# Optimization experiments

Measured on AMD Instinct MI355X. Metric: run time of the kernel, lower is better.

## Reference

```python
import jax, jax.numpy as jnp
import numpy as np

B, NN, D, H, L, E, NC = 512, 64, 128, 4, 2, 262144, 8
N = B * NN
HD = D // H


def _mlp(x, W1, b1, W2, b2):
    return jax.nn.relu(x @ W1 + b1) @ W2 + b2


def setup_inputs() -> dict:
    key = jax.random.key(0)
    ks = iter(jax.random.split(key, 64))
    w = lambda shape, s=0.02: jax.random.normal(next(ks), shape, dtype=jnp.float32) * s
    inp = {
        'node_features': jax.random.randint(next(ks), (N,), 0, NC, dtype=jnp.int32),
        'edge_index': jax.random.randint(next(ks), (2, E), 0, N, dtype=jnp.int32),
        'ptr': jnp.arange(B + 1, dtype=jnp.int32) * NN,
        'node_emb_table': w((NC, D), 1.0),
        'edge_emb': jnp.clip(jax.random.normal(next(ks), (1, D), dtype=jnp.float32), -2.0, 2.0),
        'eW1': w((L, 3 * D, D)), 'eb1': jnp.zeros((L, D)), 'eW2': w((L, D, D)), 'eb2': jnp.zeros((L, D)),
        'nW1': w((L, 3 * D, D)), 'nb1': jnp.zeros((L, D)), 'nW2': w((L, D, D)), 'nb2': jnp.zeros((L, D)),
        'gW1': w((L, 3 * D, D)), 'gb1': jnp.zeros((L, D)), 'gW2': w((L, D, D)), 'gb2': jnp.zeros((L, D)),
        'projW': w((D, 3 * D)), 'projb': jnp.zeros((3 * D,)),
        'Wq': w((D, D)), 'Wk': w((D, D)), 'Wv': w((D, D)),
        'bq': jnp.zeros((D,)), 'bk': jnp.zeros((D,)), 'bv': jnp.zeros((D,)),
        'outW': w((D, D)), 'outb': jnp.zeros((D,)),
        'sW1': w((D, D)), 'sb1': jnp.zeros((D,)), 'sW2': w((D, D)), 'sb2': jnp.zeros((D,)),
        'rW1': w((D, D)), 'rb1': jnp.zeros((D,)), 'rW2': w((D, D)), 'rb2': jnp.zeros((D,)),
        'stW1': w((D, D)), 'stb1': jnp.zeros((D,)), 'stW2': w((D, 1)), 'stb2': jnp.zeros((1,)),
        'temperature': jnp.float32(1.0),
    }
    return inp


def reference(node_features, edge_index, ptr, node_emb_table, edge_emb,
              eW1, eb1, eW2, eb2, nW1, nb1, nW2, nb2, gW1, gb1, gW2, gb2,
              projW, projb, Wq, Wk, Wv, bq, bk, bv, outW, outb,
              sW1, sb1, sW2, sb2, rW1, rb1, rW2, rb2,
              stW1, stb1, stW2, stb2, temperature):
    n_graphs = ptr.shape[0] - 1                       # static
    batch_idx = jnp.repeat(jnp.arange(n_graphs), NN)  # uniform graphs of NN nodes
    node_embs = node_emb_table[node_features]         # [N, D]
    edge_embs = jnp.broadcast_to(edge_emb, (edge_index.shape[1], D))  # [E, D]
    g = jnp.zeros((n_graphs, D), node_embs.dtype)
    src, dst = edge_index[0], edge_index[1]
    for l in range(L):
        ein = jnp.concatenate([node_embs[src], node_embs[dst], edge_embs], -1)  # [E, 3D]
        edge_embs = edge_embs + _mlp(ein, eW1[l], eb1[l], eW2[l], eb2[l])
        node_aggr = jax.ops.segment_sum(edge_embs, dst, num_segments=N)         # [N, D]
        nin = jnp.concatenate([node_embs, node_aggr, g[batch_idx]], -1)
        node_embs = node_embs + _mlp(nin, nW1[l], nb1[l], nW2[l], nb2[l])
        eg = jax.ops.segment_sum(node_aggr, batch_idx, num_segments=n_graphs)
        ng = jax.ops.segment_sum(node_embs, batch_idx, num_segments=n_graphs)
        g = g + _mlp(jnp.concatenate([ng, eg, g], -1), gW1[l], gb1[l], gW2[l], gb2[l])
    # projection + self-attention over the NN nodes of each graph
    x = node_embs.reshape(n_graphs, NN, D) @ projW + projb   # [B, NN, 3D]
    q, k, v = jnp.split(x, 3, axis=-1)
    qh = (q @ Wq + bq).reshape(n_graphs, NN, H, HD)
    kh = (k @ Wk + bk).reshape(n_graphs, NN, H, HD)
    vh = (v @ Wv + bv).reshape(n_graphs, NN, H, HD)
    scores = jnp.einsum('bqhd,bkhd->bhqk', qh, kh) / jnp.sqrt(jnp.float32(HD))
    attn = jax.nn.softmax(scores, axis=-1)
    ctx = jnp.einsum('bhqk,bkhd->bqhd', attn, vh).reshape(n_graphs, NN, D)
    a = ctx @ outW + outb
    senders = _mlp(a, sW1, sb1, sW2, sb2)
    receivers = _mlp(a, rW1, rb1, rW2, rb2)
    edge_actions = jnp.einsum('bqd,bkd->bqk', senders, receivers).reshape(n_graphs, NN * NN)
    edge_actions = edge_actions / jax.nn.softplus(temperature)
    stop = _mlp(g, stW1, stb1, stW2, stb2)[:, 0]
    at = jnp.full((n_graphs, 3), -jnp.inf, dtype=edge_actions.dtype)
    at = at.at[:, 1].set(jax.nn.log_sigmoid(-stop))   # ADD_EDGE
    at = at.at[:, 2].set(jax.nn.log_sigmoid(stop))    # EXIT
    return (at, edge_actions)
```

## Files before the change

### kernel.cpp

```cpp
#include <hip/hip_runtime.h>
#include <hip/hip_bf16.h>
#include <cstdint>
#include <cstddef>

#define D_   128
#define NN_  64
#define B_   512
#define N_   32768
#define E_   262144

typedef float4 f4;
typedef _Float16 h16;
typedef __attribute__((ext_vector_type(8))) _Float16 h16x8;
typedef __attribute__((ext_vector_type(4))) float f32x4;

__device__ __forceinline__ f4 ld4(const float* p) { return *(const f4*)p; }
__device__ __forceinline__ void st4(float* p, f4 v) { *(f4*)p = v; }

__device__ __forceinline__ int swz(int row, int slot) {
  return row * 128 + ((slot ^ (row & 7)) << 3);
}
__device__ __forceinline__ h16x8 pk8(f4 a, f4 b) {
  h16x8 v;
  v[0]=(h16)a.x; v[1]=(h16)a.y; v[2]=(h16)a.z; v[3]=(h16)a.w;
  v[4]=(h16)b.x; v[5]=(h16)b.y; v[6]=(h16)b.z; v[7]=(h16)b.w;
  return v;
}
#define MFMA16(a,b,c) __builtin_amdgcn_mfma_f32_16x16x32_f16((a),(b),(c),0,0,0)

__device__ __forceinline__ void stage_a32(const float* __restrict__ A, h16* A_s, int r0, int tid) {
  int r = tid >> 2, q = tid & 3;
  const float* Ar = A + (size_t)(r0 + r) * 128 + q * 32;
#pragma unroll
  for (int i = 0; i < 4; ++i)
    *(h16x8*)&A_s[swz(r, q * 4 + i)] = pk8(ld4(Ar + i * 8), ld4(Ar + i * 8 + 4));
}
__device__ __forceinline__ void stage_a16(const h16* __restrict__ A, h16* A_s, int r0, int tid) {
  int r = tid >> 2, q = tid & 3;
  const h16* Ar = A + (size_t)(r0 + r) * 128 + q * 32;
#pragma unroll
  for (int i = 0; i < 4; ++i)
    *(h16x8*)&A_s[swz(r, q * 4 + i)] = *(const h16x8*)(Ar + i * 8);
}
__device__ __forceinline__ void bfrag_g(const h16* __restrict__ Bt, int n0, int lq, int lr, h16x8 bf[2][4]) {
#pragma unroll
  for (int nf = 0; nf < 2; ++nf) {
    const h16* row = Bt + (size_t)(n0 + nf * 16 + lr) * 128 + lq * 8;
#pragma unroll
    for (int ks = 0; ks < 4; ++ks)
      bf[nf][ks] = *(const h16x8*)(row + ks * 32);
  }
}
__device__ __forceinline__ void mfma8(const h16* A_s, h16x8 bf[2][4], f32x4 acc[4][2], int lq, int lr) {
#pragma unroll
  for (int mf = 0; mf < 4; ++mf)
#pragma unroll
    for (int ks = 0; ks < 4; ++ks) {
      h16x8 af = *(h16x8*)&A_s[swz(mf * 16 + lr, ks * 4 + lq)];
      acc[mf][0] = MFMA16(af, bf[0][ks], acc[mf][0]);
      acc[mf][1] = MFMA16(af, bf[1][ks], acc[mf][1]);
    }
}
__device__ __forceinline__ void zacc(f32x4 acc[4][2]) {
#pragma unroll
  for (int mf = 0; mf < 4; ++mf) { acc[mf][0] = (f32x4)0.f; acc[mf][1] = (f32x4)0.f; }
}

__global__ __launch_bounds__(256)
void k_embed(const int* __restrict__ nf, const float* __restrict__ tab, float* __restrict__ out) {
  int idx = blockIdx.x * 256 + threadIdx.x;
  int row = idx >> 5, q = idx & 31;
  st4(out + (size_t)row * D_ + q * 4, ld4(tab + (size_t)nf[row] * D_ + q * 4));
}

__global__ __launch_bounds__(256)
void k_zero_cnt(int* __restrict__ cnt) { cnt[blockIdx.x * 256 + threadIdx.x] = 0; }

__global__ __launch_bounds__(256)
void k_hist(const int* __restrict__ dst, int* __restrict__ cnt) {
  atomicAdd(&cnt[dst[blockIdx.x * 256 + threadIdx.x]], 1);
}

__global__ __launch_bounds__(256)
void k_scan(const int* __restrict__ cnt, int* __restrict__ base, int* __restrict__ cursor) {
  __shared__ int sums[256];
  __shared__ int offs[256];
  const int t = threadIdx.x;
  const int start = t * 128;
  int s = 0;
  for (int i = 0; i < 128; ++i) s += cnt[start + i];
  sums[t] = s;
  __syncthreads();
  if (t == 0) { int acc = 0; for (int i = 0; i < 256; ++i) { offs[i] = acc; acc += sums[i]; } }
  __syncthreads();
  int off = offs[t];
  for (int i = 0; i < 128; ++i) { base[start + i] = off; cursor[start + i] = off; off += cnt[start + i]; }
  if (t == 255) base[N_] = off;
}

__global__ __launch_bounds__(256)
void k_scatter(const int* __restrict__ dst, int* __restrict__ cursor, int* __restrict__ eid) {
  int e = blockIdx.x * 256 + threadIdx.x;
  int p = atomicAdd(&cursor[dst[e]], 1);
  eid[p] = e;
}

__global__ __launch_bounds__(256)
void k_aggr(const h16* __restrict__ edgeb, const int* __restrict__ csrB,
            float* __restrict__ aggr) {
  const int node = blockIdx.x * 4 + (threadIdx.x >> 6);
  const int d2 = (threadIdx.x & 63) * 2;
  const int b0 = csrB[node], b1 = csrB[node + 1];
  float s0 = 0.f, s1 = 0.f;
  for (int i = b0; i < b1; ++i) {
    const h16* p = edgeb + (size_t)i * 128 + d2;
    s0 += (float)p[0]; s1 += (float)p[1];
  }
  aggr[(size_t)node * 128 + d2 + 0] = s0;
  aggr[(size_t)node * 128 + d2 + 1] = s1;
}

struct TP { const float* p[32]; };
__global__ __launch_bounds__(256)
void k_w2t(TP tp, h16* __restrict__ dst) {
  __shared__ h16 w_s[128][132];
  const float* S = tp.p[blockIdx.x];
  h16* Dd = dst + (size_t)blockIdx.x * 16384;
  const int t = threadIdx.x, r = t >> 1, hf = t & 1;
  for (int i = 0; i < 64; i += 4) {
    f4 x = ld4(S + r * 128 + hf * 64 + i);
    w_s[r][hf*64+i+0] = (h16)x.x; w_s[r][hf*64+i+1] = (h16)x.y;
    w_s[r][hf*64+i+2] = (h16)x.z; w_s[r][hf*64+i+3] = (h16)x.w;
  }
  __syncthreads();
  for (int i8 = 0; i8 < 64; i8 += 8) {
    h16x8 v;
#pragma unroll
    for (int j = 0; j < 8; ++j) v[j] = w_s[hf*64 + i8 + j][r];
    *(h16x8*)(Dd + (size_t)r * 128 + hf * 64 + i8) = v;
  }
}

__global__ __launch_bounds__(256, 2)
void k_weff(const float* __restrict__ projW, const h16* __restrict__ wt_qkv,
            h16* __restrict__ wout) {
  __shared__ h16 A_s[64 * 128];
  const int i = blockIdx.x >> 1, half = blockIdx.x & 1;
  const int r0 = half * 64;
  const int tid = threadIdx.x;
  const int lane = tid & 63, w = tid >> 6;
  const int n0 = w * 32, lq = lane >> 4, lr = lane & 15;
  stage_a16(wt_qkv + (size_t)i * 16384, A_s, r0, tid);
  __syncthreads();
  h16x8 bf[2][4];
#pragma unroll
  for (int nf = 0; nf < 2; ++nf) {
    const int r = n0 + nf * 16 + lr;
    const float* prow = projW + (size_t)r * 384 + i * 128 + lq * 8;
#pragma unroll
    for (int ks = 0; ks < 4; ++ks)
      bf[nf][ks] = pk8(ld4(prow + ks * 32), ld4(prow + ks * 32 + 4));
  }
  f32x4 acc[4][2];
  zacc(acc);
  mfma8(A_s, bf, acc, lq, lr);
  h16* Wo = wout + (size_t)i * 16384;
#pragma unroll
  for (int nf = 0; nf < 2; ++nf) {
    const int r = n0 + nf * 16 + lr;
#pragma unroll
    for (int mf = 0; mf < 4; ++mf)
#pragma unroll
      for (int reg = 0; reg < 4; ++reg)
        Wo[(size_t)(r0 + mf * 16 + lq * 4 + reg) * 128 + r] = (h16)acc[mf][nf][reg];
  }
}

__global__ __launch_bounds__(256, 2)
void k_gemm3o(const float* __restrict__ A,
              const h16* __restrict__ B1, const h16* __restrict__ B2,
              const h16* __restrict__ B3,
              const float* __restrict__ bias,
              h16* __restrict__ O1, h16* __restrict__ O2, h16* __restrict__ O3) {
  __shared__ h16 A_s[64 * 128];
  const int tid = threadIdx.x;
  const int r0 = blockIdx.x * 64;
  const int lane = tid & 63, w = tid >> 6;
  const int n0 = w * 32, lq = lane >> 4, lr = lane & 15;
  stage_a32(A, A_s, r0, tid);
  __syncthreads();
  const h16* Bs[3] = {B1, B2, B3};
  h16*       Os[3] = {O1, O2, O3};
#pragma unroll
  for (int o = 0; o < 3; ++o) {
    if (!Bs[o]) break;
    h16x8 bf[2][4];
    f32x4 acc[4][2];
    bfrag_g(Bs[o], n0, lq, lr, bf);
    zacc(acc);
    mfma8(A_s, bf, acc, lq, lr);
#pragma unroll
    for (int nf = 0; nf < 2; ++nf) {
      const int col = n0 + nf * 16 + lr;
      const float bv = bias ? bias[o * 128 + col] : 0.f;
#pragma unroll
      for (int mf = 0; mf < 4; ++mf)
#pragma unroll
        for (int reg = 0; reg < 4; ++reg)
          Os[o][(size_t)(r0 + mf * 16 + lq * 4 + reg) * 128 + col] = (h16)(acc[mf][nf][reg] + bv);
    }
  }
}

__global__ __launch_bounds__(256, 2)
void k_mlp2(const float* __restrict__ A1, const float* __restrict__ A2,
            const float* __restrict__ A3,
            const h16* __restrict__ B1a, const h16* __restrict__ B1b,
            const h16* __restrict__ B1c,
            const float* __restrict__ bias1,
            const h16* __restrict__ B2, const float* __restrict__ bias2,
            const float* __restrict__ addC,
            float* __restrict__ C) {
  __shared__ h16 A_s[64 * 128];
  const int tid = threadIdx.x;
  const int r0 = blockIdx.x * 64;
  const int lane = tid & 63, w = tid >> 6;
  const int n0 = w * 32, lq = lane >> 4, lr = lane & 15;
  h16x8 bf[2][4];
  f32x4 acc[4][2];
  zacc(acc);
  stage_a32(A1, A_s, r0, tid);
  __syncthreads();
  bfrag_g(B1a, n0, lq, lr, bf);
  mfma8(A_s, bf, acc, lq, lr);
  if (A2) {
    __syncthreads();
    stage_a32(A2, A_s, r0, tid);
    __syncthreads();
    bfrag_g(B1b, n0, lq, lr, bf);
    mfma8(A_s, bf, acc, lq, lr);
  }
  if (A3) {
    __syncthreads();
    stage_a32(A3, A_s, r0, tid);
    __syncthreads();
    bfrag_g(B1c, n0, lq, lr, bf);
    mfma8(A_s, bf, acc, lq, lr);
  }
  __syncthreads();
#pragma unroll
  for (int nf = 0; nf < 2; ++nf) {
    const int col = n0 + nf * 16 + lr;
    const float b1v = bias1 ? bias1[col] : 0.f;
#pragma unroll
    for (int mf = 0; mf < 4; ++mf)
#pragma unroll
      for (int reg = 0; reg < 4; ++reg) {
        const int row = mf * 16 + lq * 4 + reg;
        A_s[swz(row, col >> 3) + (col & 7)] = (h16)fmaxf(acc[mf][nf][reg] + b1v, 0.f);
      }
  }
  __syncthreads();
  bfrag_g(B2, n0, lq, lr, bf);
  zacc(acc);
  mfma8(A_s, bf, acc, lq, lr);
#pragma unroll
  for (int nf = 0; nf < 2; ++nf) {
    const int col = n0 + nf * 16 + lr;
    const float b2v = bias2 ? bias2[col] : 0.f;
#pragma unroll
    for (int mf = 0; mf < 4; ++mf)
#pragma unroll
      for (int reg = 0; reg < 4; ++reg) {
        const int row = r0 + mf * 16 + lq * 4 + reg;
        float x = acc[mf][nf][reg] + b2v;
        if (addC) x += addC[(size_t)row * 128 + col];
        C[(size_t)row * 128 + col] = x;
      }
  }
}

__global__ __launch_bounds__(256, 2)
void k_nodemlp(float* __restrict__ node, const float* __restrict__ aggr,
               const float* __restrict__ gbuf,
               const h16* __restrict__ B1a, const h16* __restrict__ B1b,
               const float* __restrict__ nW1c, const float* __restrict__ nb1,
               const h16* __restrict__ B2, const float* __restrict__ nb2,
               float* __restrict__ ngb, float* __restrict__ egb) {
  __shared__ h16 A_s[64 * 128];
  __shared__ float gt_s[2][128];
  __shared__ float eg_s[2][128];
  const int tid = threadIdx.x, g = blockIdx.x, r0 = g * 64;
  const int lane = tid & 63, w = tid >> 6;
  const int n0 = w * 32, lq = lane >> 4, lr = lane & 15;
  h16x8 bf[2][4];
  f32x4 acc[4][2];
  zacc(acc);
  stage_a32(node, A_s, r0, tid);
  __syncthreads();
  bfrag_g(B1a, n0, lq, lr, bf);
  mfma8(A_s, bf, acc, lq, lr);
  {
    const int col = tid & 127, half = tid >> 7;
    float s = 0.f;
    const float* gb = gbuf + (size_t)g * 128;
    for (int j = half * 64; j < half * 64 + 64; ++j)
      s += gb[j] * nW1c[(size_t)j * 128 + col];
    gt_s[half][col] = s;
  }
  __syncthreads();
  stage_a32(aggr, A_s, r0, tid);
  __syncthreads();
  bfrag_g(B1b, n0, lq, lr, bf);
  mfma8(A_s, bf, acc, lq, lr);
  {
    const int col = tid & 127, half = tid >> 7;
    float s = 0.f;
    for (int r = half * 32; r < half * 32 + 32; ++r)
      s += aggr[((size_t)r0 + r) * 128 + col];
    eg_s[half][col] = s;
  }
  __syncthreads();
#pragma unroll
  for (int nf = 0; nf < 2; ++nf) {
    const int col = n0 + nf * 16 + lr;
    const float gt = gt_s[0][col] + gt_s[1][col] + nb1[col];
#pragma unroll
    for (int mf = 0; mf < 4; ++mf)
#pragma unroll
      for (int reg = 0; reg < 4; ++reg) {
        const int row = mf * 16 + lq * 4 + reg;
        A_s[swz(row, col >> 3) + (col & 7)] = (h16)fmaxf(acc[mf][nf][reg] + gt, 0.f);
      }
  }
  if (tid < 128) egb[(size_t)g * 128 + tid] = eg_s[0][tid] + eg_s[1][tid];
  __syncthreads();
  bfrag_g(B2, n0, lq, lr, bf);
  zacc(acc);
  mfma8(A_s, bf, acc, lq, lr);
#pragma unroll
  for (int nf = 0; nf < 2; ++nf) {
    const int col = n0 + nf * 16 + lr;
    const float b2v = nb2[col];
    float cs = 0.f;
#pragma unroll
    for (int mf = 0; mf < 4; ++mf)
#pragma unroll
      for (int reg = 0; reg < 4; ++reg) {
        const int row = r0 + mf * 16 + lq * 4 + reg;
        float x = acc[mf][nf][reg] + b2v + node[(size_t)row * 128 + col];
        node[(size_t)row * 128 + col] = x;
        cs += x;
      }
    cs += __shfl_xor(cs, 16);
    cs += __shfl_xor(cs, 32);
    if (lq == 0) ngb[(size_t)g * 128 + col] = cs;
  }
}

__global__ __launch_bounds__(128)
void k_hc0(const float* __restrict__ ee, const float* __restrict__ W1c,
           const float* __restrict__ b1, float* __restrict__ hc0) {
  int j = threadIdx.x;
  float s = b1[j];
  for (int d = 0; d < 128; ++d) s += ee[d] * W1c[d * 128 + j];
  hc0[j] = s;
}

__global__ __launch_bounds__(256, 2)
void k_edge0(const int* __restrict__ src, const int* __restrict__ dst,
             const int* __restrict__ eid,
             const h16* __restrict__ hs, const h16* __restrict__ hd,
             const float* __restrict__ hc0, const h16* __restrict__ Wt2,
             const float* __restrict__ eb2, const float* __restrict__ ee,
             h16* __restrict__ edgeb) {
  __shared__ h16 H_s[64 * 128];
  __shared__ int ss[64], sd[64];
  const int tid = threadIdx.x;
  const int e0 = blockIdx.x * 64;
  const int lane = tid & 63, w = tid >> 6;
  const int n0 = w * 32, lq = lane >> 4, lr = lane & 15;
  if (tid < 64) { int e = eid[e0 + tid]; ss[tid] = src[e]; sd[tid] = dst[e]; }
  __syncthreads();
  {
    int e = tid >> 2, q = tid & 3;
    const h16* ps = hs + (size_t)ss[e] * 128 + q * 32;
    const h16* pd = hd + (size_t)sd[e] * 128 + q * 32;
#pragma unroll
    for (int i = 0; i < 4; ++i) {
      h16x8 a = *(const h16x8*)(ps + i * 8);
      h16x8 b = *(const h16x8*)(pd + i * 8);
      f4 c0 = ld4(hc0 + q * 32 + i * 8), c1 = ld4(hc0 + q * 32 + i * 8 + 4);
      h16x8 v;
      v[0]=(h16)fmaxf((float)a[0]+(float)b[0]+c0.x,0.f); v[1]=(h16)fmaxf((float)a[1]+(float)b[1]+c0.y,0.f);
      v[2]=(h16)fmaxf((float)a[2]+(float)b[2]+c0.z,0.f); v[3]=(h16)fmaxf((float)a[3]+(float)b[3]+c0.w,0.f);
      v[4]=(h16)fmaxf((float)a[4]+(float)b[4]+c1.x,0.f); v[5]=(h16)fmaxf((float)a[5]+(float)b[5]+c1.y,0.f);
      v[6]=(h16)fmaxf((float)a[6]+(float)b[6]+c1.z,0.f); v[7]=(h16)fmaxf((float)a[7]+(float)b[7]+c1.w,0.f);
      *(h16x8*)&H_s[swz(e, q * 4 + i)] = v;
    }
  }
  __syncthreads();
  h16x8 bf[2][4];
  f32x4 acc[4][2];
  bfrag_g(Wt2, n0, lq, lr, bf);
  zacc(acc);
  mfma8(H_s, bf, acc, lq, lr);
  __syncthreads();
#pragma unroll
  for (int nf = 0; nf < 2; ++nf) {
    const int col = n0 + nf * 16 + lr;
    const float base = eb2[col] + ee[col];
#pragma unroll
    for (int mf = 0; mf < 4; ++mf)
#pragma unroll
      for (int reg = 0; reg < 4; ++reg) {
        const int row = mf * 16 + lq * 4 + reg;
        H_s[swz(row, col >> 3) + (col & 7)] = (h16)(acc[mf][nf][reg] + base);
      }
  }
  __syncthreads();
  {
    int r = tid >> 2, q = tid & 3;
#pragma unroll
    for (int i = 0; i < 4; ++i) {
      int slot = q * 4 + i;
      h16x8 v = *(const h16x8*)&H_s[swz(r, slot)];
      *(h16x8*)(edgeb + (size_t)(e0 + r) * 128 + slot * 8) = v;
    }
  }
}

__global__ __launch_bounds__(256, 2)
void k_edge1(const int* __restrict__ src, const int* __restrict__ dst,
             const int* __restrict__ eid,
             h16* __restrict__ edgeb,
             const h16* __restrict__ hs, const h16* __restrict__ hd,
             const h16* __restrict__ Wt1c, const float* __restrict__ b1,
             const h16* __restrict__ Wt2, const float* __restrict__ b2) {
  __shared__ h16 T_s[64 * 128];
  __shared__ h16 HS_s[64 * 128];
  __shared__ int ss[64], sd[64];
  const int tid = threadIdx.x;
  const int e0 = blockIdx.x * 64;
  const int lane = tid & 63, w = tid >> 6;
  const int n0 = w * 32, lq = lane >> 4, lr = lane & 15;
  if (tid < 64) { int e = eid[e0 + tid]; ss[tid] = src[e]; sd[tid] = dst[e]; }
  {
    int r = tid >> 2, q = tid & 3;
    const h16* Er = edgeb + (size_t)(e0 + r) * 128 + q * 32;
#pragma unroll
    for (int i = 0; i < 4; ++i)
      *(h16x8*)&T_s[swz(r, q * 4 + i)] = *(const h16x8*)(Er + i * 8);
  }
  __syncthreads();
  {
    int e = tid >> 2, q = tid & 3;
    const h16* ps = hs + (size_t)ss[e] * 128 + q * 32;
    const h16* pd = hd + (size_t)sd[e] * 128 + q * 32;
#pragma unroll
    for (int i = 0; i < 4; ++i) {
      h16x8 a = *(const h16x8*)(ps + i * 8);
      h16x8 b = *(const h16x8*)(pd + i * 8);
      f4 c0 = ld4(b1 + q * 32 + i * 8), c1 = ld4(b1 + q * 32 + i * 8 + 4);
      h16x8 v;
      v[0]=(h16)((float)a[0]+(float)b[0]+c0.x); v[1]=(h16)((float)a[1]+(float)b[1]+c0.y);
      v[2]=(h16)((float)a[2]+(float)b[2]+c0.z); v[3]=(h16)((float)a[3]+(float)b[3]+c0.w);
      v[4]=(h16)((float)a[4]+(float)b[4]+c1.x); v[5]=(h16)((float)a[5]+(float)b[5]+c1.y);
      v[6]=(h16)((float)a[6]+(float)b[6]+c1.z); v[7]=(h16)((float)a[7]+(float)b[7]+c1.w);
      *(h16x8*)&HS_s[swz(e, q * 4 + i)] = v;
    }
  }
  h16x8 bf[2][4];
  f32x4 acc[4][2];
  bfrag_g(Wt1c, n0, lq, lr, bf);
  zacc(acc);
  mfma8(T_s, bf, acc, lq, lr);
  float rres[2][4][4];
#pragma unroll
  for (int nf = 0; nf < 2; ++nf) {
    const int col = n0 + nf * 16 + lr;
#pragma unroll
    for (int mf = 0; mf < 4; ++mf)
#pragma unroll
      for (int reg = 0; reg < 4; ++reg) {
        const int row = mf * 16 + lq * 4 + reg;
        rres[nf][mf][reg] = (float)T_s[swz(row, col >> 3) + (col & 7)];
      }
  }
  __syncthreads();
#pragma unroll
  for (int nf = 0; nf < 2; ++nf) {
    const int col = n0 + nf * 16 + lr;
#pragma unroll
    for (int mf = 0; mf < 4; ++mf)
#pragma unroll
      for (int reg = 0; reg < 4; ++reg) {
        const int row = mf * 16 + lq * 4 + reg;
        float x = acc[mf][nf][reg] + (float)HS_s[swz(row, col >> 3) + (col & 7)];
        T_s[swz(row, col >> 3) + (col & 7)] = (h16)fmaxf(x, 0.f);
      }
  }
  __syncthreads();
  bfrag_g(Wt2, n0, lq, lr, bf);
  zacc(acc);
  mfma8(T_s, bf, acc, lq, lr);
#pragma unroll
  for (int nf = 0; nf < 2; ++nf) {
    const int col = n0 + nf * 16 + lr;
    const float b2v = b2[col];
#pragma unroll
    for (int mf = 0; mf < 4; ++mf)
#pragma unroll
      for (int reg = 0; reg < 4; ++reg) {
        const int row = mf * 16 + lq * 4 + reg;
        HS_s[swz(row, col >> 3) + (col & 7)] = (h16)(acc[mf][nf][reg] + b2v + rres[nf][mf][reg]);
      }
  }
  __syncthreads();
  {
    int r = tid >> 2, q = tid & 3;
#pragma unroll
    for (int i = 0; i < 4; ++i) {
      int slot = q * 4 + i;
      h16x8 v = *(const h16x8*)&HS_s[swz(r, slot)];
      *(h16x8*)(edgeb + (size_t)(e0 + r) * 128 + slot * 8) = v;
    }
  }
}

__global__ __launch_bounds__(128)
void k_beff(const float* __restrict__ projb,
            const float* __restrict__ Wq, const float* __restrict__ Wk, const float* __restrict__ Wv,
            const float* __restrict__ bq, const float* __restrict__ bk, const float* __restrict__ bv,
            float* __restrict__ beff) {
  int i = blockIdx.x, k = threadIdx.x;
  const float* W = (i == 0) ? Wq : ((i == 1) ? Wk : Wv);
  const float* bb = (i == 0) ? bq : ((i == 1) ? bk : bv);
  float s = bb[k];
  for (int j = 0; j < 128; ++j) s += projb[i * 128 + j] * W[j * 128 + k];
  beff[i * 128 + k] = s;
}

__global__ __launch_bounds__(256, 2)
void k_qkv_attn(const float* __restrict__ node_in,
                const h16* __restrict__ Wq_t, const h16* __restrict__ Wk_t,
                const h16* __restrict__ Wv_t, const float* __restrict__ beff,
                const h16* __restrict__ outWt, const float* __restrict__ outb,
                float* __restrict__ nodeOut) {
  __shared__ h16 A_s[64 * 128];
  __shared__ h16 q_s[64][136];
  __shared__ h16 k_s[64][136];
  __shared__ h16 v_s[64][136];
  const int tid = threadIdx.x, g = blockIdx.x, r0 = g * 64;
  const int lane = tid & 63, w = tid >> 6;
  const int n0 = w * 32, lq = lane >> 4, lr = lane & 15;
  stage_a32(node_in, A_s, r0, tid);
  __syncthreads();
  const h16* Ws[3] = {Wq_t, Wk_t, Wv_t};
#pragma unroll
  for (int o = 0; o < 3; ++o) {
    h16x8 bf[2][4];
    f32x4 acc[4][2];
    bfrag_g(Ws[o], n0, lq, lr, bf);
    zacc(acc);
    mfma8(A_s, bf, acc, lq, lr);
#pragma unroll
    for (int nf = 0; nf < 2; ++nf) {
      const int col = n0 + nf * 16 + lr;
      const float bv = beff[o * 128 + col];
#pragma unroll
      for (int mf = 0; mf < 4; ++mf)
#pragma unroll
        for (int reg = 0; reg < 4; ++reg) {
          const int row = mf * 16 + lq * 4 + reg;
          h16 x = (h16)(acc[mf][nf][reg] + bv);
          if (o == 0) q_s[row][col] = x;
          else if (o == 1) k_s[row][col] = x;
          else v_s[row][col] = x;
        }
    }
  }
  __syncthreads();
  const int co = n0;
  h16x8 qv[4];
#pragma unroll
  for (int j = 0; j < 4; ++j)
    qv[j] = *(const h16x8*)&q_s[lane][co + j * 8];
  float s[64];
  const float scale = 0.17677669529663688f;
#pragma unroll 8
  for (int k = 0; k < 64; ++k) {
    float a = 0.f;
#pragma unroll
    for (int j = 0; j < 4; ++j) {
      h16x8 k8 = *(const h16x8*)&k_s[k][co + j * 8];
#pragma unroll
      for (int t = 0; t < 8; ++t) a += (float)qv[j][t] * (float)k8[t];
    }
    s[k] = a * scale;
  }
  float m = s[0];
#pragma unroll
  for (int k = 1; k < 64; ++k) m = fmaxf(m, s[k]);
  float sum = 0.f;
#pragma unroll
  for (int k = 0; k < 64; ++k) { s[k] = expf(s[k] - m); sum += s[k]; }
  const float inv = 1.f / sum;
  f4 cv[8];
#pragma unroll
  for (int jj = 0; jj < 8; ++jj) cv[jj] = make_float4(0.f, 0.f, 0.f, 0.f);
#pragma unroll 4
  for (int k = 0; k < 64; ++k) {
    float p = s[k];
#pragma unroll
    for (int j = 0; j < 4; ++j) {
      h16x8 v8 = *(const h16x8*)&v_s[k][co + j * 8];
      cv[2*j].x   += p * (float)v8[0]; cv[2*j].y   += p * (float)v8[1];
      cv[2*j].z   += p * (float)v8[2]; cv[2*j].w   += p * (float)v8[3];
      cv[2*j+1].x += p * (float)v8[4]; cv[2*j+1].y += p * (float)v8[5];
      cv[2*j+1].z += p * (float)v8[6]; cv[2*j+1].w += p * (float)v8[7];
    }
  }
#pragma unroll
  for (int jj = 0; jj < 4; ++jj) {
    f4 a = cv[2*jj], b = cv[2*jj+1];
    a.x *= inv; a.y *= inv; a.z *= inv; a.w *= inv;
    b.x *= inv; b.y *= inv; b.z *= inv; b.w *= inv;
    *(h16x8*)&A_s[swz(lane, (co >> 3) + jj)] = pk8(a, b);
  }
  __syncthreads();
  h16x8 bf[2][4];
  f32x4 acc[4][2];
  bfrag_g(outWt, n0, lq, lr, bf);
  zacc(acc);
  mfma8(A_s, bf, acc, lq, lr);
  const size_t base = (size_t)r0 * 128;
#pragma unroll
  for (int nf = 0; nf < 2; ++nf) {
    const int col = n0 + nf * 16 + lr;
    const float bv = outb[col];
#pragma unroll
    for (int mf = 0; mf < 4; ++mf)
#pragma unroll
      for (int reg = 0; reg < 4; ++reg)
        nodeOut[base + (size_t)(mf * 16 + lq * 4 + reg) * 128 + col] = acc[mf][nf][reg] + bv;
  }
}

__global__ __launch_bounds__(256, 2)
void k_sr_edgeact(const float* __restrict__ node_in,
                  const h16* __restrict__ sW1t, const float* __restrict__ sb1,
                  const h16* __restrict__ sW2t, const float* __restrict__ sb2,
                  const h16* __restrict__ rW1t, const float* __restrict__ rb1,
                  const h16* __restrict__ rW2t, const float* __restrict__ rb2,
                  const float* __restrict__ temp, float* __restrict__ out) {
  __shared__ h16 A_s[64 * 128];
  __shared__ h16 H_s[64 * 128];
  __shared__ h16 S_s[64 * 128];
  __shared__ h16 R_s[64][136];
  const int tid = threadIdx.x, g = blockIdx.x, r0 = g * 64;
  const int lane = tid & 63, w = tid >> 6;
  const int n0 = w * 32, lq = lane >> 4, lr = lane & 15;
  stage_a32(node_in, A_s, r0, tid);
  __syncthreads();
  h16x8 bf[2][4];
  f32x4 acc[4][2];
  bfrag_g(sW1t, n0, lq, lr, bf);
  zacc(acc);
  mfma8(A_s, bf, acc, lq, lr);
#pragma unroll
  for (int nf = 0; nf < 2; ++nf) {
    const int col = n0 + nf * 16 + lr;
    const float b1v = sb1[col];
#pragma unroll
    for (int mf = 0; mf < 4; ++mf)
#pragma unroll
      for (int reg = 0; reg < 4; ++reg) {
        const int row = mf * 16 + lq * 4 + reg;
        H_s[swz(row, col >> 3) + (col & 7)] = (h16)fmaxf(acc[mf][nf][reg] + b1v, 0.f);
      }
  }
  __syncthreads();
  bfrag_g(sW2t, n0, lq, lr, bf);
  zacc(acc);
  mfma8(H_s, bf, acc, lq, lr);
#pragma unroll
  for (int nf = 0; nf < 2; ++nf) {
    const int col = n0 + nf * 16 + lr;
    const float b2v = sb2[col];
#pragma unroll
    for (int mf = 0; mf < 4; ++mf)
#pragma unroll
      for (int reg = 0; reg < 4; ++reg) {
        const int row = mf * 16 + lq * 4 + reg;
        S_s[swz(row, col >> 3) + (col & 7)] = (h16)(acc[mf][nf][reg] + b2v);
      }
  }
  __syncthreads();
  bfrag_g(rW1t, n0, lq, lr, bf);
  zacc(acc);
  mfma8(A_s, bf, acc, lq, lr);
#pragma unroll
  for (int nf = 0; nf < 2; ++nf) {
    const int col = n0 + nf * 16 + lr;
    const float b1v = rb1[col];
#pragma unroll
    for (int mf = 0; mf < 4; ++mf)
#pragma unroll
      for (int reg = 0; reg < 4; ++reg) {
        const int row = mf * 16 + lq * 4 + reg;
        H_s[swz(row, col >> 3) + (col & 7)] = (h16)fmaxf(acc[mf][nf][reg] + b1v, 0.f);
      }
  }
  __syncthreads();
  bfrag_g(rW2t, n0, lq, lr, bf);
  zacc(acc);
  mfma8(H_s, bf, acc, lq, lr);
#pragma unroll
  for (int nf = 0; nf < 2; ++nf) {
    const int col = n0 + nf * 16 + lr;
    const float b2v = rb2[col];
#pragma unroll
    for (int mf = 0; mf < 4; ++mf)
#pragma unroll
      for (int reg = 0; reg < 4; ++reg) {
        const int row = mf * 16 + lq * 4 + reg;
        R_s[row][col] = (h16)(acc[mf][nf][reg] + b2v);
      }
  }
  __syncthreads();
  const int n0e = w * 16;
  h16x8 bfR[4];
#pragma unroll
  for (int ks = 0; ks < 4; ++ks)
    bfR[ks] = *(const h16x8*)&R_s[n0e + lr][lq * 8 + ks * 32];
  f32x4 acc4[4];
#pragma unroll
  for (int mf = 0; mf < 4; ++mf) acc4[mf] = (f32x4)0.f;
#pragma unroll
  for (int mf = 0; mf < 4; ++mf)
#pragma unroll
    for (int ks = 0; ks < 4; ++ks) {
      h16x8 af = *(h16x8*)&S_s[swz(mf * 16 + lr, ks * 4 + lq)];
      acc4[mf] = MFMA16(af, bfR[ks], acc4[mf]);
    }
  const float inv = 1.f / log1pf(expf(temp[0]));
  __syncthreads();
  float* O_s = (float*)H_s;
#pragma unroll
  for (int mf = 0; mf < 4; ++mf)
#pragma unroll
    for (int reg = 0; reg < 4; ++reg)
      O_s[(mf * 16 + lq * 4 + reg) * 64 + n0e + lr] = acc4[mf][reg] * inv;
  __syncthreads();
#pragma unroll
  for (int i = 0; i < 4; ++i)
    st4(out + (size_t)g * 4096 + tid * 16 + i * 4, *(const f4*)&O_s[tid * 16 + i * 4]);
}

__global__ __launch_bounds__(256, 2)
void k_stophead(const float* __restrict__ gbuf, const h16* __restrict__ stW1t,
                const float* __restrict__ stb1, const float* __restrict__ stW2,
                const float* __restrict__ stb2, float* __restrict__ out) {
  __shared__ h16 A_s[64 * 128];
  __shared__ h16 H_s[64 * 128];
  const int tid = threadIdx.x, r0 = blockIdx.x * 64;
  const int lane = tid & 63, w = tid >> 6;
  const int n0 = w * 32, lq = lane >> 4, lr = lane & 15;
  stage_a32(gbuf, A_s, r0, tid);
  __syncthreads();
  h16x8 bf[2][4];
  f32x4 acc[4][2];
  bfrag_g(stW1t, n0, lq, lr, bf);
  zacc(acc);
  mfma8(A_s, bf, acc, lq, lr);
#pragma unroll
  for (int nf = 0; nf < 2; ++nf) {
    const int col = n0 + nf * 16 + lr;
    const float b1v = stb1[col];
#pragma unroll
    for (int mf = 0; mf < 4; ++mf)
#pragma unroll
      for (int reg = 0; reg < 4; ++reg) {
        const int row = mf * 16 + lq * 4 + reg;
        H_s[swz(row, col >> 3) + (col & 7)] = (h16)fmaxf(acc[mf][nf][reg] + b1v, 0.f);
      }
  }
  __syncthreads();
  if (tid < 64) {
    float s = stb2[0];
    for (int c = 0; c < 128; ++c)
      s += (float)H_s[swz(tid, c >> 3) + (c & 7)] * stW2[c];
    float l = log1pf(expf(-fabsf(s)));
    int b = r0 + tid;
    out[b * 3 + 0] = -3.3895313892515355e38f;
    out[b * 3 + 1] = fminf(-s, 0.f) - l;
    out[b * 3 + 2] = fminf(s, 0.f) - l;
  }
}

static const size_t OFF_NODE  = 0;
static const size_t OFF_HSRC  = 4194304;
static const size_t OFF_HDST  = 8388608;
static const size_t OFF_AGGR  = 12582912;
static const size_t OFF_G     = 20971520;
static const size_t OFF_NG    = OFF_G + 65536;
static const size_t OFF_EG    = OFF_NG + 65536;
static const size_t OFF_BEFF  = OFF_EG + 65536;
static const size_t OFF_HC0   = OFF_BEFF + 384;
static const size_t OFF_EDGE  = 21495808;
static const size_t OFF_CSR   = OFF_EDGE + (size_t)E_ * 128;
static const size_t CSR_INTS  = (size_t)N_ + (N_ + 1) + N_ + E_;
static const size_t OFF_WT    = OFF_CSR + ((CSR_INTS + 63) & ~(size_t)63) / 1 / 4 * 4 + 64;

#define WT_WQ 0
#define WT_WK 1
#define WT_WV 2
#define WT_OUTW 3
#define WT_SW1 4
#define WT_SW2 5
#define WT_RW1 6
#define WT_RW2 7
#define WT_STW1 8
#define WT_L(l,i) (9 + (l)*11 + (i))
#define WT_EW1C1 31
#define WT_WEFF 32
#define WTP(i) (wt + (size_t)(i) * 16384)

extern "C" void kernel_launch(void* const* d_in, const int* in_sizes, int n_in,
                              void* d_out, int out_size, void* d_ws, size_t ws_size,
                              hipStream_t stream) {
  (void)in_sizes; (void)n_in; (void)out_size; (void)ws_size;
  const int*   nf    = (const int*)d_in[0];
  const int*   ei    = (const int*)d_in[1];
  const float* tab   = (const float*)d_in[3];
  const float* ee    = (const float*)d_in[4];
  const float* eW1   = (const float*)d_in[5];
  const float* eb1   = (const float*)d_in[6];
  const float* eW2   = (const float*)d_in[7];
  const float* eb2   = (const float*)d_in[8];
  const float* nW1   = (const float*)d_in[9];
  const float* nb1   = (const float*)d_in[10];
  const float* nW2   = (const float*)d_in[11];
  const float* nb2   = (const float*)d_in[12];
  const float* gW1   = (const float*)d_in[13];
  const float* gb1   = (const float*)d_in[14];
  const float* gW2   = (const float*)d_in[15];
  const float* gb2   = (const float*)d_in[16];
  const float* projW = (const float*)d_in[17];
  const float* projb = (const float*)d_in[18];
  const float* Wq    = (const float*)d_in[19];
  const float* Wk    = (const float*)d_in[20];
  const float* Wv    = (const float*)d_in[21];
  const float* bq    = (const float*)d_in[22];
  const float* bk    = (const float*)d_in[23];
  const float* bv    = (const float*)d_in[24];
  const float* outW  = (const float*)d_in[25];
  const float* outb  = (const float*)d_in[26];
  const float* sW1   = (const float*)d_in[27];
  const float* sb1   = (const float*)d_in[28];
  const float* sW2   = (const float*)d_in[29];
  const float* sb2   = (const float*)d_in[30];
  const float* rW1   = (const float*)d_in[31];
  const float* rb1   = (const float*)d_in[32];
  const float* rW2   = (const float*)d_in[33];
  const float* rb2   = (const float*)d_in[34];
  const float* stW1  = (const float*)d_in[35];
  const float* stb1  = (const float*)d_in[36];
  const float* stW2  = (const float*)d_in[37];
  const float* stb2  = (const float*)d_in[38];
  const float* temp  = (const float*)d_in[39];

  const int* srcI = ei;
  const int* dstI = ei + E_;

  float* ws    = (float*)d_ws;
  float* node  = ws + OFF_NODE;
  float* hsrcF = ws + OFF_HSRC;
  float* hdstF = ws + OFF_HDST;
  float* aggr  = ws + OFF_AGGR;
  float* gbuf  = ws + OFF_G;
  float* ngb   = ws + OFF_NG;
  float* egb   = ws + OFF_EG;
  float* beff  = ws + OFF_BEFF;
  float* hc0   = ws + OFF_HC0;
  h16*  hsrcH  = (h16*)hsrcF;
  h16*  hdstH  = (h16*)hdstF;
  h16*  edgebH = (h16*)(ws + OFF_EDGE);
  int* cnt    = (int*)(ws + OFF_CSR);
  int* csrB   = cnt + N_;
  int* cursor = csrB + (N_ + 1);
  int* eidL   = cursor + N_;
  h16* wt     = (h16*)(ws + OFF_WT);
  float* outp = (float*)d_out;

  hipMemsetAsync(gbuf, 0, (size_t)B_ * D_ * sizeof(float), stream);
  k_embed<<<4096, 256, 0, stream>>>(nf, tab, node);

  k_zero_cnt<<<N_ / 256, 256, 0, stream>>>(cnt);
  k_hist<<<E_ / 256, 256, 0, stream>>>(dstI, cnt);
  k_scan<<<1, 256, 0, stream>>>(cnt, csrB, cursor);
  k_scatter<<<E_ / 256, 256, 0, stream>>>(dstI, cursor, eidL);

  TP tp;
  tp.p[WT_WQ] = Wq; tp.p[WT_WK] = Wk; tp.p[WT_WV] = Wv; tp.p[WT_OUTW] = outW;
  tp.p[WT_SW1] = sW1; tp.p[WT_SW2] = sW2; tp.p[WT_RW1] = rW1; tp.p[WT_RW2] = rW2;
  tp.p[WT_STW1] = stW1;
  for (int l = 0; l < 2; ++l) {
    tp.p[WT_L(l,0)]  = eW1 + (size_t)l * 384 * 128;
    tp.p[WT_L(l,1)]  = eW1 + (size_t)l * 384 * 128 + 128 * 128;
    tp.p[WT_L(l,2)]  = eW2 + (size_t)l * 128 * 128;
    tp.p[WT_L(l,3)]  = nW1 + (size_t)l * 384 * 128;
    tp.p[WT_L(l,4)]  = nW1 + (size_t)l * 384 * 128 + 128 * 128;
    tp.p[WT_L(l,5)]  = nW1 + (size_t)l * 384 * 128 + 256 * 128;
    tp.p[WT_L(l,6)]  = nW2 + (size_t)l * 128 * 128;
    tp.p[WT_L(l,7)]  = gW1 + (size_t)l * 384 * 128;
    tp.p[WT_L(l,8)]  = gW1 + (size_t)l * 384 * 128 + 128 * 128;
    tp.p[WT_L(l,9)]  = gW1 + (size_t)l * 384 * 128 + 256 * 128;
    tp.p[WT_L(l,10)] = gW2 + (size_t)l * 128 * 128;
  }
  tp.p[WT_EW1C1] = eW1 + (size_t)384 * 128 + 256 * 128;
  k_w2t<<<32, 256, 0, stream>>>(tp, wt);

  k_weff<<<6, 256, 0, stream>>>(projW, WTP(WT_WQ), WTP(WT_WEFF));
  k_beff<<<3, 128, 0, stream>>>(projb, Wq, Wk, Wv, bq, bk, bv, beff);

  for (int l = 0; l < 2; ++l) {
    const float* eb1l = eb1 + l * 128;
    const float* eb2l = eb2 + l * 128;
    const float* nb1l = nb1 + l * 128;
    const float* nb2l = nb2 + l * 128;
    const float* gb1l = gb1 + l * 128;
    const float* gb2l = gb2 + l * 128;
    const float* nW1cl = nW1 + (size_t)l * 384 * 128 + 256 * 128;

    k_gemm3o<<<N_ / 64, 256, 0, stream>>>(node, WTP(WT_L(l,0)), WTP(WT_L(l,1)), nullptr,
                                          nullptr, hsrcH, hdstH, nullptr);
    if (l == 0) {
      k_hc0<<<1, 128, 0, stream>>>(ee, eW1 + 256 * 128, eb1l, hc0);
      k_edge0<<<E_ / 64, 256, 0, stream>>>(srcI, dstI, eidL, hsrcH, hdstH, hc0,
                                           WTP(WT_L(0,2)), eb2l, ee, edgebH);
    } else {
      k_edge1<<<E_ / 64, 256, 0, stream>>>(srcI, dstI, eidL, edgebH, hsrcH, hdstH,
                                           WTP(WT_EW1C1), eb1l, WTP(WT_L(1,2)), eb2l);
    }
    k_aggr<<<N_ / 4, 256, 0, stream>>>(edgebH, csrB, aggr);
    k_nodemlp<<<B_, 256, 0, stream>>>(node, aggr, gbuf,
                                      WTP(WT_L(l,3)), WTP(WT_L(l,4)),
                                      nW1cl, nb1l,
                                      WTP(WT_L(l,6)), nb2l, ngb, egb);
    k_mlp2<<<B_ / 64, 256, 0, stream>>>(ngb, egb, gbuf,
                                        WTP(WT_L(l,7)), WTP(WT_L(l,8)), WTP(WT_L(l,9)),
                                        gb1l,
                                        WTP(WT_L(l,10)), gb2l, gbuf, gbuf);
  }

  k_qkv_attn<<<B_, 256, 0, stream>>>(node, WTP(WT_WEFF + 0), WTP(WT_WEFF + 1),
                                     WTP(WT_WEFF + 2), beff, WTP(WT_OUTW), outb, node);
  k_sr_edgeact<<<B_, 256, 0, stream>>>(node,
                                       WTP(WT_SW1), sb1, WTP(WT_SW2), sb2,
                                       WTP(WT_RW1), rb1, WTP(WT_RW2), rb2,
                                       temp, outp + 3 * B_);
  k_stophead<<<B_ / 64, 256, 0, stream>>>(gbuf, WTP(WT_STW1), stb1, stW2, stb2, outp);
}
```

Measured before the change: 431.0 us.

## Fuse per-node edge aggregation into edge MLP kernels via segmented reduction

Removes the separate k_aggr pass that reread all edge features from global memory. Each edge-MLP block now runs a segmented sum over its dst-sorted rows from shared memory. It writes directly when a node's edge run lies entirely inside the block and uses atomicAdd otherwise, so a memset of aggr is added each layer. The layer-1 kernel also drops its final edge-feature writeback, since nothing reads it afterwards. The cost is float atomics and a serial 32-row loop per thread in the epilogue.

```diff
diff --git a/kernel.cpp b/kernel.cpp
--- a/kernel.cpp
+++ b/kernel.cpp
@@ -64,6 +64,28 @@
 __device__ __forceinline__ void zacc(f32x4 acc[4][2]) {
 #pragma unroll
   for (int mf = 0; mf < 4; ++mf) { acc[mf][0] = (f32x4)0.f; acc[mf][1] = (f32x4)0.f; }
+}
+
+__device__ __forceinline__ void aggr_epilogue(const h16* T, const int* sd,
+                                              const int* __restrict__ csrB,
+                                              float* __restrict__ aggr,
+                                              int e0, int tid) {
+  const int col = tid & 127;
+  const int rbeg = (tid >> 7) * 32, rend = rbeg + 32;
+  float s = 0.f;
+  int v = sd[rbeg], runA = rbeg;
+  for (int r = rbeg; r < rend; ++r) {
+    s += (float)T[swz(r, col >> 3) + (col & 7)];
+    int nv = (r + 1 < rend) ? sd[r + 1] : -1;
+    if (nv != v) {
+      int gb = csrB[v], ge = csrB[v + 1];
+      if (gb == e0 + runA && ge == e0 + r + 1)
+        aggr[(size_t)v * 128 + col] = s;
+      else
+        atomicAdd(&aggr[(size_t)v * 128 + col], s);
+      s = 0.f; v = nv; runA = r + 1;
+    }
+  }
 }
 
 __global__ __launch_bounds__(256)
@@ -103,21 +125,6 @@
   int e = blockIdx.x * 256 + threadIdx.x;
   int p = atomicAdd(&cursor[dst[e]], 1);
   eid[p] = e;
-}
-
-__global__ __launch_bounds__(256)
-void k_aggr(const h16* __restrict__ edgeb, const int* __restrict__ csrB,
-            float* __restrict__ aggr) {
-  const int node = blockIdx.x * 4 + (threadIdx.x >> 6);
-  const int d2 = (threadIdx.x & 63) * 2;
-  const int b0 = csrB[node], b1 = csrB[node + 1];
-  float s0 = 0.f, s1 = 0.f;
-  for (int i = b0; i < b1; ++i) {
-    const h16* p = edgeb + (size_t)i * 128 + d2;
-    s0 += (float)p[0]; s1 += (float)p[1];
-  }
-  aggr[(size_t)node * 128 + d2 + 0] = s0;
-  aggr[(size_t)node * 128 + d2 + 1] = s1;
 }
 
 struct TP { const float* p[32]; };
@@ -369,11 +376,11 @@
 
 __global__ __launch_bounds__(256, 2)
 void k_edge0(const int* __restrict__ src, const int* __restrict__ dst,
-             const int* __restrict__ eid,
+             const int* __restrict__ eid, const int* __restrict__ csrB,
              const h16* __restrict__ hs, const h16* __restrict__ hd,
              const float* __restrict__ hc0, const h16* __restrict__ Wt2,
              const float* __restrict__ eb2, const float* __restrict__ ee,
-             h16* __restrict__ edgeb) {
+             h16* __restrict__ edgeb, float* __restrict__ aggr) {
   __shared__ h16 H_s[64 * 128];
   __shared__ int ss[64], sd[64];
   const int tid = threadIdx.x;
@@ -428,15 +435,17 @@
       *(h16x8*)(edgeb + (size_t)(e0 + r) * 128 + slot * 8) = v;
     }
   }
+  aggr_epilogue(H_s, sd, csrB, aggr, e0, tid);
 }
 
 __global__ __launch_bounds__(256, 2)
 void k_edge1(const int* __restrict__ src, const int* __restrict__ dst,
-             const int* __restrict__ eid,
-             h16* __restrict__ edgeb,
+             const int* __restrict__ eid, const int* __restrict__ csrB,
+             const h16* __restrict__ edgeb,
              const h16* __restrict__ hs, const h16* __restrict__ hd,
              const h16* __restrict__ Wt1c, const float* __restrict__ b1,
-             const h16* __restrict__ Wt2, const float* __restrict__ b2) {
+             const h16* __restrict__ Wt2, const float* __restrict__ b2,
+             float* __restrict__ aggr) {
   __shared__ h16 T_s[64 * 128];
   __shared__ h16 HS_s[64 * 128];
   __shared__ int ss[64], sd[64];
@@ -517,15 +526,7 @@
       }
   }
   __syncthreads();
-  {
-    int r = tid >> 2, q = tid & 3;
-#pragma unroll
-    for (int i = 0; i < 4; ++i) {
-      int slot = q * 4 + i;
-      h16x8 v = *(const h16x8*)&HS_s[swz(r, slot)];
-      *(h16x8*)(edgeb + (size_t)(e0 + r) * 128 + slot * 8) = v;
-    }
-  }
+  aggr_epilogue(HS_s, sd, csrB, aggr, e0, tid);
 }
 
 __global__ __launch_bounds__(128)
@@ -936,15 +937,15 @@
 
     k_gemm3o<<<N_ / 64, 256, 0, stream>>>(node, WTP(WT_L(l,0)), WTP(WT_L(l,1)), nullptr,
                                           nullptr, hsrcH, hdstH, nullptr);
+    hipMemsetAsync(aggr, 0, (size_t)N_ * D_ * sizeof(float), stream);
     if (l == 0) {
       k_hc0<<<1, 128, 0, stream>>>(ee, eW1 + 256 * 128, eb1l, hc0);
-      k_edge0<<<E_ / 64, 256, 0, stream>>>(srcI, dstI, eidL, hsrcH, hdstH, hc0,
-                                           WTP(WT_L(0,2)), eb2l, ee, edgebH);
+      k_edge0<<<E_ / 64, 256, 0, stream>>>(srcI, dstI, eidL, csrB, hsrcH, hdstH, hc0,
+                                           WTP(WT_L(0,2)), eb2l, ee, edgebH, aggr);
     } else {
-      k_edge1<<<E_ / 64, 256, 0, stream>>>(srcI, dstI, eidL, edgebH, hsrcH, hdstH,
-                                           WTP(WT_EW1C1), eb1l, WTP(WT_L(1,2)), eb2l);
-    }
-    k_aggr<<<N_ / 4, 256, 0, stream>>>(edgebH, csrB, aggr);
+      k_edge1<<<E_ / 64, 256, 0, stream>>>(srcI, dstI, eidL, csrB, edgebH, hsrcH, hdstH,
+                                           WTP(WT_EW1C1), eb1l, WTP(WT_L(1,2)), eb2l, aggr);
+    }
     k_nodemlp<<<B_, 256, 0, stream>>>(node, aggr, gbuf,
                                       WTP(WT_L(l,3)), WTP(WT_L(l,4)),
                                       nW1cl, nb1l,
```

Measured after the change: 448.5 us. 1.04x slower.
